# Kernel tuning notes

Hardware: AMD Instinct MI355X
Metric: run time of the kernel (lower is better)

Reference implementation:

```python
import jax, jax.numpy as jnp
import numpy as np

B, S, D = 16, 2048, 1024   # batch, src_len, per-tensor feature dim (input_dim*growth_factor)
OUT = 1024                 # output_dim


def setup_inputs() -> dict:
    key = jax.random.key(0)
    k1, k2, k3, k4, k5, k6 = jax.random.split(key, 6)
    hidden = jax.random.normal(k1, (B, S, D), dtype=jnp.float32)
    encoder_outputs = jax.random.normal(k2, (B, S, D), dtype=jnp.float32)
    c_t = jax.random.normal(k3, (B, D), dtype=jnp.float32)
    # Linear(input_dim*3*growth_factor=3*D, OUT): PyTorch stores weight as [OUT, 3D]
    limit = 1.0 / np.sqrt(3 * D)
    W = jax.random.uniform(k4, (OUT, 3 * D), minval=-limit, maxval=limit, dtype=jnp.float32)
    b = jax.random.uniform(k5, (OUT,), minval=-limit, maxval=limit, dtype=jnp.float32)
    v = jax.random.uniform(k6, (OUT,), dtype=jnp.float32)  # torch.rand -> U[0,1)
    return {"hidden": hidden, "encoder_outputs": encoder_outputs, "c_t": c_t,
            "W": W, "b": b, "v": v}


def reference(hidden, encoder_outputs, c_t, W, b, v):
    # c_t broadcast over src_len; concat on feature dim -> [B, S, 3D]
    c_rep = jnp.broadcast_to(c_t[:, None, :], hidden.shape)
    cat = jnp.concatenate((hidden, c_rep, encoder_outputs), axis=2)
    # energy = relu(cat @ W^T + b): [B, S, OUT]
    energy = jax.nn.relu(jnp.einsum('bsf,of->bso', cat, W) + b)
    # attention = energy @ v: [B, S], then softmax over src_len
    attention = jnp.einsum('bso,o->bs', energy, v)
    return jax.nn.softmax(attention, axis=1)
```

## Files before the change

kernel.cpp:

```cpp
#include <hip/hip_runtime.h>
#include <hip/hip_bf16.h>


typedef __attribute__((ext_vector_type(8))) short short8;
typedef __attribute__((ext_vector_type(4))) float f32x4;
typedef __attribute__((ext_vector_type(8))) unsigned short ushort8v;
typedef __attribute__((ext_vector_type(4))) unsigned short ushort4v;

#define NB 16
#define NS 2048
#define ND 1024
#define NOUT 1024
#define NM (NB * NS)
#define KHE 2048

#define B8M 256
#define B8N 256
#define B8K 64
#define NT8 (KHE / B8K)

#define PREP_ACONV 16384
#define PREP_WCONV 2048
#define PREP_CBIAS 256
#define PREP_ZERO 32

__device__ __forceinline__ unsigned short bf16_rne(float x) {
    unsigned int u = __float_as_uint(x);
    unsigned int r = (u + 0x7fffu + ((u >> 16) & 1u)) >> 16;
    return (unsigned short)r;
}

__global__ __launch_bounds__(256) void prep_k(const float* __restrict__ hidden,
                                              const float* __restrict__ enc,
                                              const float* __restrict__ c_t,
                                              const float* __restrict__ W,
                                              const float* __restrict__ bias,
                                              unsigned short* __restrict__ Abf,
                                              unsigned short* __restrict__ Wbf,
                                              float* __restrict__ cbias,
                                              float* __restrict__ logits) {
    const int bid = blockIdx.x;
    const int tid = threadIdx.x;
    if (bid < PREP_ACONV) {
        size_t c = (size_t)bid * 256 + tid;
        size_t m = c >> 7;
        int k = (int)(c & 127) * 16;
        const float* src = (k < ND) ? (hidden + m * ND + k) : (enc + m * ND + (k - ND));
        float4 f0 = ((const float4*)src)[0];
        float4 f1 = ((const float4*)src)[1];
        float4 f2 = ((const float4*)src)[2];
        float4 f3 = ((const float4*)src)[3];
        ushort8v h0, h1;
        h0[0] = bf16_rne(f0.x); h0[1] = bf16_rne(f0.y); h0[2] = bf16_rne(f0.z); h0[3] = bf16_rne(f0.w);
        h0[4] = bf16_rne(f1.x); h0[5] = bf16_rne(f1.y); h0[6] = bf16_rne(f1.z); h0[7] = bf16_rne(f1.w);
        h1[0] = bf16_rne(f2.x); h1[1] = bf16_rne(f2.y); h1[2] = bf16_rne(f2.z); h1[3] = bf16_rne(f2.w);
        h1[4] = bf16_rne(f3.x); h1[5] = bf16_rne(f3.y); h1[6] = bf16_rne(f3.z); h1[7] = bf16_rne(f3.w);
        *(ushort8v*)(Abf + m * KHE + k) = h0;
        *(ushort8v*)(Abf + m * KHE + k + 8) = h1;
    } else if (bid < PREP_ACONV + PREP_WCONV) {
        int idx = (bid - PREP_ACONV) * 256 + tid;
        int o = idx >> 9;
        int k = (idx & 511) * 4;
        int off = (k < ND) ? k : (k + ND);
        float4 f = *(const float4*)(W + (size_t)o * 3072 + off);
        ushort4v h;
        h.x = bf16_rne(f.x); h.y = bf16_rne(f.y); h.z = bf16_rne(f.z); h.w = bf16_rne(f.w);
        *(ushort4v*)(Wbf + (size_t)o * KHE + k) = h;
    } else if (bid < PREP_ACONV + PREP_WCONV + PREP_CBIAS) {
        int o = (bid - PREP_ACONV - PREP_WCONV) * 4 + (tid >> 6);
        int lane = tid & 63;
        const float* w = W + (size_t)o * 3072 + ND;
        float wr[16];
        #pragma unroll
        for (int j = 0; j < 16; ++j) wr[j] = w[lane + j * 64];
        float bo = bias[o];
        for (int b = 0; b < NB; ++b) {
            const float* cc = c_t + (size_t)b * ND;
            float s = 0.f;
            #pragma unroll
            for (int j = 0; j < 16; ++j) s = fmaf(cc[lane + j * 64], wr[j], s);
            #pragma unroll
            for (int m = 1; m < 64; m <<= 1) s += __shfl_xor(s, m);
            if (lane == 0) cbias[b * NOUT + o] = s + bo;
        }
    } else {
        int idx = (bid - PREP_ACONV - PREP_WCONV - PREP_CBIAS) * 256 + tid;
        ((float4*)logits)[idx] = make_float4(0.f, 0.f, 0.f, 0.f);
    }
}

__global__ __launch_bounds__(256) void wconv_k(const float* __restrict__ W,
                                               unsigned short* __restrict__ Wbf) {
    int idx = blockIdx.x * 256 + threadIdx.x;
    int o = idx >> 9;
    int k = (idx & 511) * 4;
    int off = (k < ND) ? k : (k + ND);
    float4 f = *(const float4*)(W + (size_t)o * 3072 + off);
    ushort4v h;
    h.x = bf16_rne(f.x); h.y = bf16_rne(f.y); h.z = bf16_rne(f.z); h.w = bf16_rne(f.w);
    *(ushort4v*)(Wbf + (size_t)o * KHE + k) = h;
}

__global__ __launch_bounds__(256) void cbias_k(const float* __restrict__ c_t,
                                               const float* __restrict__ W,
                                               const float* __restrict__ bias,
                                               float* __restrict__ cbias) {
    int o = blockIdx.x * 4 + (threadIdx.x >> 6);
    int lane = threadIdx.x & 63;
    const float* w = W + (size_t)o * 3072 + ND;
    float wr[16];
    #pragma unroll
    for (int j = 0; j < 16; ++j) wr[j] = w[lane + j * 64];
    float bo = bias[o];
    for (int b = 0; b < NB; ++b) {
        const float* c = c_t + (size_t)b * ND;
        float s = 0.f;
        #pragma unroll
        for (int j = 0; j < 16; ++j) s = fmaf(c[lane + j * 64], wr[j], s);
        #pragma unroll
        for (int m = 1; m < 64; m <<= 1) s += __shfl_xor(s, m);
        if (lane == 0) cbias[b * NOUT + o] = s + bo;
    }
}

__global__ __launch_bounds__(512, 2) void gemm8_k(const unsigned short* __restrict__ Abf,
                                                  const unsigned short* __restrict__ Wbf,
                                                  const float* __restrict__ cbias,
                                                  const float* __restrict__ v,
                                                  float* __restrict__ logits) {
    __shared__ unsigned short Ls[2][512][B8K] __attribute__((aligned(16)));
    __shared__ float rowsum[4][B8M];
    __shared__ float cb_s[B8N];
    __shared__ float v_s[B8N];

    const int tid = threadIdx.x;
    const int ntile = blockIdx.x & 3;
    const int mtile = blockIdx.x >> 2;
    const int m0 = mtile * B8M;
    const int o0 = ntile * B8N;
    const int batch = m0 >> 11;

    if (tid < B8N) {
        cb_s[tid] = cbias[batch * NOUT + o0 + tid];
        v_s[tid] = v[o0 + tid];
    }

    const int wid = tid >> 6;
    const int lane = tid & 63;
    const int wm = (wid & 1) * 128;
    const int wn = (wid >> 1) * 64;
    const int lr = lane >> 3;
    const int lc = (lane & 7) ^ lr;

    f32x4 acc[8][4] = {};

    auto gload = [&](int c, int kt) -> ushort8v {
        if (c < 4) {
            const int r0 = c * 64 + wid * 8;
            return *(const ushort8v*)(Abf + (size_t)(m0 + r0 + lr) * KHE + kt + lc * 8);
        } else {
            const int r0 = (c - 4) * 64 + wid * 8;
            return *(const ushort8v*)(Wbf + (size_t)(o0 + r0 + lr) * KHE + kt + lc * 8);
        }
    };
    auto swrite = [&](unsigned short* bufp, int c, ushort8v val) {
        const int r0 = ((c < 4) ? c * 64 : 256 + (c - 4) * 64) + wid * 8;
        *(ushort8v*)(bufp + (size_t)(r0 + lr) * B8K + (lane & 7) * 8) = val;
    };
    auto loadAf = [&](const unsigned short* bufp, int mh, int ks, short8* d) {
        const int cb = ks * 4 + (lane >> 4);
        #pragma unroll
        for (int i = 0; i < 4; ++i) {
            const int row = wm + mh * 64 + i * 16 + (lane & 15);
            d[i] = *(const short8*)(bufp + (size_t)row * B8K + (cb ^ (row & 7)) * 8);
        }
    };
    auto loadBf = [&](const unsigned short* bufp, int nh, int ks, short8* d) {
        const int cb = ks * 4 + (lane >> 4);
        #pragma unroll
        for (int j = 0; j < 2; ++j) {
            const int row = 256 + wn + nh * 32 + j * 16 + (lane & 15);
            d[j] = *(const short8*)(bufp + (size_t)row * B8K + (cb ^ (row & 7)) * 8);
        }
    };
    auto mfma8 = [&](int mh, int nh, const short8* a4, const short8* b2) {
        __builtin_amdgcn_s_setprio(1);
        #pragma unroll
        for (int i = 0; i < 4; ++i)
            #pragma unroll
            for (int j = 0; j < 2; ++j)
                acc[mh * 4 + i][nh * 2 + j] = __builtin_amdgcn_mfma_f32_16x16x32_bf16(
                    a4[i], b2[j], acc[mh * 4 + i][nh * 2 + j], 0, 0, 0);
        __builtin_amdgcn_s_setprio(0);
    };

    unsigned short* curp = &Ls[0][0][0];
    unsigned short* nxtp = &Ls[1][0][0];

    {
        ushort8v g[8];
        #pragma unroll
        for (int c = 0; c < 8; ++c) g[c] = gload(c, 0);
        #pragma unroll
        for (int c = 0; c < 8; ++c) swrite(curp, c, g[c]);
    }
    asm volatile("s_waitcnt lgkmcnt(0)" ::: "memory");
    __builtin_amdgcn_s_barrier();
    asm volatile("" ::: "memory");

    #pragma unroll 1
    for (int t = 0; t < NT8; ++t) {
        const int kt1 = (t + 1) * B8K;
        const bool pf = (t + 1 < NT8);
        short8 aA[4], aB[4], aC[4], aD[4], bA[2], bB[2], bC[2], bD[2];
        ushort8v g0[4], g1[4];

        if (pf) {
            #pragma unroll
            for (int c = 0; c < 4; ++c) g0[c] = gload(c, kt1);
        }
        loadAf(curp, 0, 0, aA);
        loadBf(curp, 0, 0, bA);
        loadBf(curp, 1, 0, bB);
        mfma8(0, 0, aA, bA);
        loadAf(curp, 1, 0, aB);
        mfma8(0, 1, aA, bB);
        loadAf(curp, 1, 1, aC);
        loadBf(curp, 0, 1, bC);
        mfma8(1, 1, aB, bB);
        loadBf(curp, 1, 1, bD);
        loadAf(curp, 0, 1, aD);
        if (pf) {
            #pragma unroll
            for (int c = 0; c < 4; ++c) g1[c] = gload(c + 4, kt1);
        }
        mfma8(1, 0, aB, bA);
        if (pf) { swrite(nxtp, 0, g0[0]); swrite(nxtp, 1, g0[1]); }
        mfma8(1, 0, aC, bC);
        if (pf) { swrite(nxtp, 2, g0[2]); swrite(nxtp, 3, g0[3]); }
        mfma8(1, 1, aC, bD);
        if (pf) { swrite(nxtp, 4, g1[0]); swrite(nxtp, 5, g1[1]); }
        mfma8(0, 1, aD, bD);
        if (pf) { swrite(nxtp, 6, g1[2]); swrite(nxtp, 7, g1[3]); }
        mfma8(0, 0, aD, bC);

        asm volatile("s_waitcnt lgkmcnt(0)" ::: "memory");
        __builtin_amdgcn_s_barrier();
        asm volatile("" ::: "memory");
        unsigned short* tp = curp; curp = nxtp; nxtp = tp;
    }

    __syncthreads();

    const int col = lane & 15;
    const int q = lane >> 4;
    float vv[4], cbv[4];
    #pragma unroll
    for (int j = 0; j < 4; ++j) {
        const int oc = wn + j * 16 + col;
        vv[j] = v_s[oc];
        cbv[j] = cb_s[oc];
    }
    #pragma unroll
    for (int i = 0; i < 8; ++i) {
        #pragma unroll
        for (int r = 0; r < 4; ++r) {
            float s = 0.f;
            #pragma unroll
            for (int j = 0; j < 4; ++j) {
                float e = acc[i][j][r] + cbv[j];
                e = fmaxf(e, 0.f);
                s = fmaf(e, vv[j], s);
            }
            s += __shfl_xor(s, 1);
            s += __shfl_xor(s, 2);
            s += __shfl_xor(s, 4);
            s += __shfl_xor(s, 8);
            if (col == 0) rowsum[wid >> 1][wm + i * 16 + q * 4 + r] = s;
        }
    }
    __syncthreads();
    if (tid < B8M)
        atomicAdd(&logits[m0 + tid],
                  rowsum[0][tid] + rowsum[1][tid] + rowsum[2][tid] + rowsum[3][tid]);
}

__global__ __launch_bounds__(256) void gemm_att_k(const float* __restrict__ hidden,
                                                  const float* __restrict__ enc,
                                                  const unsigned short* __restrict__ Wbf,
                                                  const float* __restrict__ Wf,
                                                  const float* __restrict__ cbias,
                                                  const float* __restrict__ v,
                                                  float* __restrict__ logits,
                                                  int use_wbf) {
    __shared__ unsigned short As[128 * 32] __attribute__((aligned(16)));
    __shared__ unsigned short Bs[128 * 32] __attribute__((aligned(16)));
    __shared__ float rowsum[2][128];
    __shared__ float cb_s[128];
    __shared__ float v_s[128];

    const int tid = threadIdx.x;
    const int ntile = blockIdx.x & 7;
    const int mtile = blockIdx.x >> 3;
    const int m0 = mtile * 128;
    const int o0 = ntile * 128;
    const int batch = m0 >> 11;

    if (tid < 128) {
        cb_s[tid] = cbias[batch * NOUT + o0 + tid];
        v_s[tid] = v[o0 + tid];
    }

    const int wid = tid >> 6;
    const int lane = tid & 63;
    const int wm = (wid & 1) * 64;
    const int wn = (wid >> 1) * 64;

    f32x4 acc[4][4] = {};

    for (int kt = 0; kt < KHE; kt += 32) {
        const float* Abase = (kt < ND) ? hidden : enc;
        const int aoff = (kt < ND) ? kt : (kt - ND);
        #pragma unroll
        for (int i = 0; i < 4; ++i) {
            int p = tid + i * 256;
            int row = p >> 3, kc = p & 7;
            float4 f = *(const float4*)(Abase + (size_t)(m0 + row) * ND + aoff + kc * 4);
            ushort4v h;
            h.x = bf16_rne(f.x); h.y = bf16_rne(f.y); h.z = bf16_rne(f.z); h.w = bf16_rne(f.w);
            *(ushort4v*)(As + row * 32 + kc * 4) = h;
        }
        if (use_wbf) {
            #pragma unroll
            for (int i = 0; i < 2; ++i) {
                int u = tid + i * 256;
                int ol = u >> 2, kc = u & 3;
                ushort8v w8 = *(const ushort8v*)(Wbf + (size_t)(o0 + ol) * KHE + kt + kc * 8);
                *(ushort8v*)(Bs + ol * 32 + kc * 8) = w8;
            }
        } else {
            const int woff = (kt < ND) ? kt : (kt + ND);
            #pragma unroll
            for (int i = 0; i < 4; ++i) {
                int p = tid + i * 256;
                int row = p >> 3, kc = p & 7;
                float4 f = *(const float4*)(Wf + (size_t)(o0 + row) * 3072 + woff + kc * 4);
                ushort4v h;
                h.x = bf16_rne(f.x); h.y = bf16_rne(f.y); h.z = bf16_rne(f.z); h.w = bf16_rne(f.w);
                *(ushort4v*)(Bs + row * 32 + kc * 4) = h;
            }
        }
        __syncthreads();

        short8 a_frag[4], b_frag[4];
        #pragma unroll
        for (int i = 0; i < 4; ++i)
            a_frag[i] = *(const short8*)(As + (wm + i * 16 + (lane & 15)) * 32 + (lane >> 4) * 8);
        #pragma unroll
        for (int j = 0; j < 4; ++j)
            b_frag[j] = *(const short8*)(Bs + (wn + j * 16 + (lane & 15)) * 32 + (lane >> 4) * 8);
        #pragma unroll
        for (int i = 0; i < 4; ++i)
            #pragma unroll
            for (int j = 0; j < 4; ++j)
                acc[i][j] = __builtin_amdgcn_mfma_f32_16x16x32_bf16(a_frag[i], b_frag[j],
                                                                    acc[i][j], 0, 0, 0);
        __syncthreads();
    }

    const int col = lane & 15;
    const int q = lane >> 4;
    float vv[4], cbv[4];
    #pragma unroll
    for (int j = 0; j < 4; ++j) {
        int oc = wn + j * 16 + col;
        vv[j] = v_s[oc];
        cbv[j] = cb_s[oc];
    }
    #pragma unroll
    for (int i = 0; i < 4; ++i) {
        #pragma unroll
        for (int r = 0; r < 4; ++r) {
            float s = 0.f;
            #pragma unroll
            for (int j = 0; j < 4; ++j) {
                float e = acc[i][j][r] + cbv[j];
                e = fmaxf(e, 0.f);
                s = fmaf(e, vv[j], s);
            }
            s += __shfl_xor(s, 1);
            s += __shfl_xor(s, 2);
            s += __shfl_xor(s, 4);
            s += __shfl_xor(s, 8);
            if (col == 0) rowsum[wid >> 1][wm + i * 16 + q * 4 + r] = s;
        }
    }
    __syncthreads();
    if (tid < 128) atomicAdd(&logits[m0 + tid], rowsum[0][tid] + rowsum[1][tid]);
}

__global__ __launch_bounds__(256) void softmax_k(const float* __restrict__ logits,
                                                 float* __restrict__ out) {
    const int b = blockIdx.x;
    const int tid = threadIdx.x;
    const int lane = tid & 63, wid = tid >> 6;
    __shared__ float redmax[4];
    __shared__ float redsum[4];
    const float* L = logits + (size_t)b * NS;
    float x[8];
    float mx = -3.4e38f;
    #pragma unroll
    for (int i = 0; i < 8; ++i) {
        x[i] = L[tid + i * 256];
        mx = fmaxf(mx, x[i]);
    }
    #pragma unroll
    for (int m = 1; m < 64; m <<= 1) mx = fmaxf(mx, __shfl_xor(mx, m));
    if (lane == 0) redmax[wid] = mx;
    __syncthreads();
    mx = fmaxf(fmaxf(redmax[0], redmax[1]), fmaxf(redmax[2], redmax[3]));
    float sum = 0.f;
    #pragma unroll
    for (int i = 0; i < 8; ++i) {
        x[i] = expf(x[i] - mx);
        sum += x[i];
    }
    #pragma unroll
    for (int m = 1; m < 64; m <<= 1) sum += __shfl_xor(sum, m);
    if (lane == 0) redsum[wid] = sum;
    __syncthreads();
    float inv = 1.0f / (redsum[0] + redsum[1] + redsum[2] + redsum[3]);
    #pragma unroll
    for (int i = 0; i < 8; ++i) out[(size_t)b * NS + tid + i * 256] = x[i] * inv;
}

extern "C" void kernel_launch(void* const* d_in, const int* in_sizes, int n_in,
                              void* d_out, int out_size, void* d_ws, size_t ws_size,
                              hipStream_t stream) {
    const float* hidden = (const float*)d_in[0];
    const float* enc    = (const float*)d_in[1];
    const float* c_t    = (const float*)d_in[2];
    const float* W      = (const float*)d_in[3];
    const float* bias   = (const float*)d_in[4];
    const float* v      = (const float*)d_in[5];
    float* out = (float*)d_out;

    char* ws = (char*)d_ws;
    float* logits = (float*)ws;
    float* cbias  = (float*)(ws + 131072);
    unsigned short* Wbf = (unsigned short*)(ws + 196608);
    unsigned short* Abf = (unsigned short*)(ws + 196608 + 4194304);
    const size_t need_wbf = 196608 + (size_t)NOUT * KHE * 2;
    const size_t need_abf = need_wbf + (size_t)NM * KHE * 2;

    if (ws_size >= need_abf) {
        prep_k<<<PREP_ACONV + PREP_WCONV + PREP_CBIAS + PREP_ZERO, 256, 0, stream>>>(
            hidden, enc, c_t, W, bias, Abf, Wbf, cbias, logits);
        gemm8_k<<<(NM / B8M) * (NOUT / B8N), 512, 0, stream>>>(Abf, Wbf, cbias, v, logits);
    } else if (ws_size >= need_wbf) {
        hipMemsetAsync(logits, 0, NM * sizeof(float), stream);
        cbias_k<<<NOUT / 4, 256, 0, stream>>>(c_t, W, bias, cbias);
        wconv_k<<<(NOUT * KHE / 4) / 256, 256, 0, stream>>>(W, Wbf);
        gemm_att_k<<<(NM / 128) * (NOUT / 128), 256, 0, stream>>>(hidden, enc, Wbf, W, cbias, v,
                                                                  logits, 1);
    } else {
        hipMemsetAsync(logits, 0, NM * sizeof(float), stream);
        cbias_k<<<NOUT / 4, 256, 0, stream>>>(c_t, W, bias, cbias);
        gemm_att_k<<<(NM / 128) * (NOUT / 128), 256, 0, stream>>>(hidden, enc, Wbf, W, cbias, v,
                                                                  logits, 0);
    }
    softmax_k<<<NB, 256, 0, stream>>>(logits, out);
}
```

Before: 426.6 us.

## Stage W tiles via direct global-to-LDS loads and unroll k-loop by two

Loads of the weight (B) tile now go straight from global memory into LDS through global_load_lds, skipping the trip through registers and the LDS write. The activation tile keeps the register path. The k-loop is manually unrolled by two with fixed ping-pong buffers, and the MFMA/LDS-read order is changed to use fewer live fragments. This is meant to cut VGPR pressure and LDS-store instructions. The trade-off is a full vmcnt(0) wait at every k-step barrier, and the B-tile swizzle now depends on the lane layout that global_load_lds produces.

Result: slower. 527.7 us (+23.7%).

```diff
diff --git a/kernel.cpp b/kernel.cpp
--- a/kernel.cpp
+++ b/kernel.cpp
@@ -28,6 +28,12 @@
     unsigned int u = __float_as_uint(x);
     unsigned int r = (u + 0x7fffu + ((u >> 16) & 1u)) >> 16;
     return (unsigned short)r;
+}
+
+__device__ __forceinline__ void gload_lds16(const unsigned short* g, unsigned short* l) {
+    __builtin_amdgcn_global_load_lds(
+        (const __attribute__((address_space(1))) void*)g,
+        (__attribute__((address_space(3))) void*)l, 16, 0, 0);
 }
 
 __global__ __launch_bounds__(256) void prep_k(const float* __restrict__ hidden,
@@ -150,24 +156,28 @@
     const int wm = (wid & 1) * 128;
     const int wn = (wid >> 1) * 64;
     const int lr = lane >> 3;
-    const int lc = (lane & 7) ^ lr;
+    const int lslot = lane & 7;
+    const int lchunk = lslot ^ lr;
 
     f32x4 acc[8][4] = {};
 
-    auto gload = [&](int c, int kt) -> ushort8v {
-        if (c < 4) {
-            const int r0 = c * 64 + wid * 8;
-            return *(const ushort8v*)(Abf + (size_t)(m0 + r0 + lr) * KHE + kt + lc * 8);
-        } else {
-            const int r0 = (c - 4) * 64 + wid * 8;
-            return *(const ushort8v*)(Wbf + (size_t)(o0 + r0 + lr) * KHE + kt + lc * 8);
-        }
-    };
-    auto swrite = [&](unsigned short* bufp, int c, ushort8v val) {
-        const int r0 = ((c < 4) ? c * 64 : 256 + (c - 4) * 64) + wid * 8;
-        *(ushort8v*)(bufp + (size_t)(r0 + lr) * B8K + (lane & 7) * 8) = val;
-    };
-    auto loadAf = [&](const unsigned short* bufp, int mh, int ks, short8* d) {
+    auto gloadA = [&](int c, int kt) -> ushort8v {
+        const int r = c * 64 + wid * 8 + lr;
+        return *(const ushort8v*)(Abf + (size_t)(m0 + r) * KHE + kt + lchunk * 8);
+    };
+    auto swriteA = [&](unsigned short* bufp, int c, ushort8v val) {
+        const int r = c * 64 + wid * 8 + lr;
+        *(ushort8v*)(bufp + (size_t)r * B8K + lslot * 8) = val;
+    };
+    auto stageB = [&](unsigned short* bufp, int kt) {
+        #pragma unroll
+        for (int t = 0; t < 4; ++t) {
+            const int r0 = wid * 32 + t * 8;
+            gload_lds16(Wbf + (size_t)(o0 + r0 + lr) * KHE + kt + lchunk * 8,
+                        bufp + (size_t)(256 + r0) * B8K);
+        }
+    };
+    auto rdA = [&](const unsigned short* bufp, int mh, int ks, short8* d) {
         const int cb = ks * 4 + (lane >> 4);
         #pragma unroll
         for (int i = 0; i < 4; ++i) {
@@ -175,7 +185,7 @@
             d[i] = *(const short8*)(bufp + (size_t)row * B8K + (cb ^ (row & 7)) * 8);
         }
     };
-    auto loadBf = [&](const unsigned short* bufp, int nh, int ks, short8* d) {
+    auto rdB = [&](const unsigned short* bufp, int nh, int ks, short8* d) {
         const int cb = ks * 4 + (lane >> 4);
         #pragma unroll
         for (int j = 0; j < 2; ++j) {
@@ -183,7 +193,7 @@
             d[j] = *(const short8*)(bufp + (size_t)row * B8K + (cb ^ (row & 7)) * 8);
         }
     };
-    auto mfma8 = [&](int mh, int nh, const short8* a4, const short8* b2) {
+    auto mm8 = [&](const short8* a4, const short8* b2, int mh, int nh) {
         __builtin_amdgcn_s_setprio(1);
         #pragma unroll
         for (int i = 0; i < 4; ++i)
@@ -194,60 +204,52 @@
         __builtin_amdgcn_s_setprio(0);
     };
 
-    unsigned short* curp = &Ls[0][0][0];
-    unsigned short* nxtp = &Ls[1][0][0];
+    unsigned short* L0 = &Ls[0][0][0];
+    unsigned short* L1 = &Ls[1][0][0];
 
     {
-        ushort8v g[8];
-        #pragma unroll
-        for (int c = 0; c < 8; ++c) g[c] = gload(c, 0);
-        #pragma unroll
-        for (int c = 0; c < 8; ++c) swrite(curp, c, g[c]);
-    }
-    asm volatile("s_waitcnt lgkmcnt(0)" ::: "memory");
-    __builtin_amdgcn_s_barrier();
-    asm volatile("" ::: "memory");
-
-    #pragma unroll 1
-    for (int t = 0; t < NT8; ++t) {
-        const int kt1 = (t + 1) * B8K;
-        const bool pf = (t + 1 < NT8);
-        short8 aA[4], aB[4], aC[4], aD[4], bA[2], bB[2], bC[2], bD[2];
-        ushort8v g0[4], g1[4];
-
-        if (pf) {
-            #pragma unroll
-            for (int c = 0; c < 4; ++c) g0[c] = gload(c, kt1);
-        }
-        loadAf(curp, 0, 0, aA);
-        loadBf(curp, 0, 0, bA);
-        loadBf(curp, 1, 0, bB);
-        mfma8(0, 0, aA, bA);
-        loadAf(curp, 1, 0, aB);
-        mfma8(0, 1, aA, bB);
-        loadAf(curp, 1, 1, aC);
-        loadBf(curp, 0, 1, bC);
-        mfma8(1, 1, aB, bB);
-        loadBf(curp, 1, 1, bD);
-        loadAf(curp, 0, 1, aD);
-        if (pf) {
-            #pragma unroll
-            for (int c = 0; c < 4; ++c) g1[c] = gload(c + 4, kt1);
-        }
-        mfma8(1, 0, aB, bA);
-        if (pf) { swrite(nxtp, 0, g0[0]); swrite(nxtp, 1, g0[1]); }
-        mfma8(1, 0, aC, bC);
-        if (pf) { swrite(nxtp, 2, g0[2]); swrite(nxtp, 3, g0[3]); }
-        mfma8(1, 1, aC, bD);
-        if (pf) { swrite(nxtp, 4, g1[0]); swrite(nxtp, 5, g1[1]); }
-        mfma8(0, 1, aD, bD);
-        if (pf) { swrite(nxtp, 6, g1[2]); swrite(nxtp, 7, g1[3]); }
-        mfma8(0, 0, aD, bC);
-
-        asm volatile("s_waitcnt lgkmcnt(0)" ::: "memory");
+        ushort8v g0 = gloadA(0, 0), g1 = gloadA(1, 0), g2 = gloadA(2, 0), g3 = gloadA(3, 0);
+        stageB(L0, 0);
+        swriteA(L0, 0, g0); swriteA(L0, 1, g1); swriteA(L0, 2, g2); swriteA(L0, 3, g3);
+        asm volatile("s_waitcnt vmcnt(0) lgkmcnt(0)" ::: "memory");
         __builtin_amdgcn_s_barrier();
         asm volatile("" ::: "memory");
-        unsigned short* tp = curp; curp = nxtp; nxtp = tp;
+    }
+
+    auto ktile = [&](unsigned short* curp, unsigned short* nxtp, int ktn, bool pf) {
+        short8 a0[4], a1[4], b0[2], b1[2];
+        ushort8v g0, g1, g2, g3;
+        if (pf) {
+            g0 = gloadA(0, ktn); g1 = gloadA(1, ktn); g2 = gloadA(2, ktn); g3 = gloadA(3, ktn);
+            stageB(nxtp, ktn);
+        }
+        rdA(curp, 0, 0, a0);
+        rdB(curp, 0, 0, b0);
+        rdB(curp, 1, 0, b1);
+        mm8(a0, b0, 0, 0);
+        rdA(curp, 1, 0, a1);
+        mm8(a0, b1, 0, 1);
+        mm8(a1, b0, 1, 0);
+        mm8(a1, b1, 1, 1);
+        rdA(curp, 0, 1, a0);
+        rdB(curp, 0, 1, b0);
+        rdB(curp, 1, 1, b1);
+        if (pf) { swriteA(nxtp, 0, g0); swriteA(nxtp, 1, g1); }
+        mm8(a0, b0, 0, 0);
+        rdA(curp, 1, 1, a1);
+        if (pf) { swriteA(nxtp, 2, g2); swriteA(nxtp, 3, g3); }
+        mm8(a0, b1, 0, 1);
+        mm8(a1, b0, 1, 0);
+        mm8(a1, b1, 1, 1);
+        asm volatile("s_waitcnt vmcnt(0) lgkmcnt(0)" ::: "memory");
+        __builtin_amdgcn_s_barrier();
+        asm volatile("" ::: "memory");
+    };
+
+    #pragma unroll 1
+    for (int it = 0; it < NT8 / 2; ++it) {
+        ktile(L0, L1, (2 * it + 1) * B8K, true);
+        ktile(L1, L0, (2 * it + 2) * B8K, it != NT8 / 2 - 1);
     }
 
     __syncthreads();
```
